# Performance work log

Measured on AMD Instinct MI355X. Metric: run time of the kernel, lower is better.

The kernel has to match this reference:

```python
import jax, jax.numpy as jnp
import numpy as np
import math

B, N, E, H = 2, 10000, 160000, 128
ET = 8
EPS = 1e-5


def setup_inputs() -> dict:
    key = jax.random.key(0)
    ks = jax.random.split(key, 20)
    s = 1.0 / math.sqrt(H)
    inp = {
        "hidden": jax.random.normal(ks[0], (B, N, H), jnp.float32),
        "time_emb": jax.random.normal(ks[1], (B, N, H), jnp.float32),
        "edge_index": jax.random.randint(ks[2], (2, E), 0, N),
        "edge_type": jax.random.randint(ks[3], (E,), 0, ET),
        # parameters
        "edge_emb": jax.random.normal(ks[4], (ET, H), jnp.float32),
        "Wq": jax.random.normal(ks[5], (H, H), jnp.float32) * s,
        "bq": jnp.zeros((H,), jnp.float32),
        "Wk": jax.random.normal(ks[6], (H, H), jnp.float32) * s,
        "bk": jnp.zeros((H,), jnp.float32),
        "Wv": jax.random.normal(ks[7], (H, H), jnp.float32) * s,
        "bv": jnp.zeros((H,), jnp.float32),
        "We": jax.random.normal(ks[8], (H, 1), jnp.float32) * s,
        "be": jnp.zeros((1,), jnp.float32),
        "W1": jax.random.normal(ks[9], (3 * H, H), jnp.float32) * (1.0 / math.sqrt(3 * H)),
        "b1": jnp.zeros((H,), jnp.float32),
        "W2": jax.random.normal(ks[10], (H, H), jnp.float32) * s,
        "b2": jnp.zeros((H,), jnp.float32),
        "gamma": jnp.ones((H,), jnp.float32),
        "beta": jnp.zeros((H,), jnp.float32),
    }
    return inp


def _forward(hidden, time_emb, edge_index, edge_type, edge_emb,
             Wq, bq, Wk, bk, Wv, bv, We, be, W1, b1, W2, b2, gamma, beta):
    src, tgt = edge_index[0], edge_index[1]
    # edge-wise gathers: [B, E, H]
    src_h = hidden[:, src]
    tgt_h = hidden[:, tgt]
    src_t = time_emb[:, src]
    tgt_t = time_emb[:, tgt]
    edge_h = edge_emb[edge_type][None, :, :]  # [1, E, H] broadcasts over batch

    query = (tgt_h + tgt_t) @ Wq + bq
    key = (src_h + src_t + edge_h) @ Wk + bk
    value = (src_h + edge_h) @ Wv + bv

    logits = jnp.einsum("beh,beh->be", query, key) / math.sqrt(H)
    logits = logits + (edge_h @ We + be)[..., 0]  # edge bias broadcast over batch

    # segment softmax per target node (equivalent to the per-node masked softmax loop)
    lT = logits.T  # [E, B]
    seg_max = jax.ops.segment_max(lT, tgt, num_segments=N)          # [N, B]
    seg_max = jnp.where(jnp.isfinite(seg_max), seg_max, 0.0)
    ex = jnp.exp(lT - seg_max[tgt])                                  # [E, B]
    seg_sum = jax.ops.segment_sum(ex, tgt, num_segments=N)           # [N, B]
    weights = (ex / seg_sum[tgt]).T                                  # [B, E]

    messages = value * weights[..., None]                            # [B, E, H]
    # scatter-add to target nodes
    agg = jax.ops.segment_sum(jnp.swapaxes(messages, 0, 1), tgt, num_segments=N)  # [N, B, H]
    aggregated = jnp.swapaxes(agg, 0, 1)                             # [B, N, H]

    cat = jnp.concatenate([hidden, aggregated, time_emb], axis=-1)   # [B, N, 3H]
    updated = jax.nn.silu(cat @ W1 + b1) @ W2 + b2

    x = hidden + updated  # dropout p=0 -> identity
    mu = jnp.mean(x, axis=-1, keepdims=True)
    var = jnp.var(x, axis=-1, keepdims=True)
    return (x - mu) * jax.lax.rsqrt(var + EPS) * gamma + beta


def reference(hidden, time_emb, edge_index, edge_type, edge_emb,
              Wq, bq, Wk, bk, Wv, bv, We, be, W1, b1, W2, b2, gamma, beta):
    return _forward(hidden, time_emb, edge_index, edge_type, edge_emb,
                    Wq, bq, Wk, bk, Wv, bv, We, be, W1, b1, W2, b2, gamma, beta)
```

## Files before the change

### kernel.cpp

```cpp
#include <hip/hip_runtime.h>
#include <math.h>

constexpr int B_  = 2;
constexpr int N_  = 10000;
constexpr int E_  = 160000;
constexpr int H_  = 128;
constexpr int ET_ = 8;
constexpr int CAP_ = 64;
constexpr float EPS_ = 1e-5f;
constexpr float RSQH = 0.08838834764831845f;

typedef __bf16 bf16x8 __attribute__((ext_vector_type(8)));
typedef short  short8 __attribute__((ext_vector_type(8)));
typedef float  f32x4  __attribute__((ext_vector_type(4)));
typedef unsigned short u16;

__device__ inline u16 bf16b(float f) {
    return __builtin_bit_cast(u16, (__bf16)f);
}

__device__ inline bf16x8 ldfrag(const u16* __restrict__ W, int kc, int nt, int lane) {
    short8 s = *(const short8*)(W + ((kc * 8 + nt) * 64 + lane) * 8);
    return __builtin_bit_cast(bf16x8, s);
}

__global__ __launch_bounds__(256)
void setup_kernel(const float* __restrict__ W1, const float* __restrict__ W2,
                  const float* __restrict__ Wq, const float* __restrict__ Wk,
                  const float* __restrict__ Wv,
                  u16* __restrict__ W1s, u16* __restrict__ W2s,
                  u16* __restrict__ Wqs, u16* __restrict__ Wks, u16* __restrict__ Wvs,
                  const float* __restrict__ edge_emb,
                  const float* __restrict__ bk, const float* __restrict__ bv,
                  const float* __restrict__ We, const float* __restrict__ be,
                  float* __restrict__ Kt, float* __restrict__ Vt, float* __restrict__ eb,
                  int* __restrict__ count)
{
    const int bid = blockIdx.x, tid = threadIdx.x;
    if (bid < 56) {
        int unit = bid >> 1, half = bid & 1;
        const float* src; u16* dst; int kc;
        if (unit < 12)      { src = W1; dst = W1s; kc = unit; }
        else if (unit < 16) { src = W2; dst = W2s; kc = unit - 12; }
        else if (unit < 20) { src = Wq; dst = Wqs; kc = unit - 16; }
        else if (unit < 24) { src = Wk; dst = Wks; kc = unit - 20; }
        else                { src = Wv; dst = Wvs; kc = unit - 24; }
        int nt = half * 4 + (tid >> 6), lane = tid & 63;
        int q = lane >> 4, c = lane & 15;
        int kbase = kc * 32 + q * 8;
        int col = nt * 16 + c;
        u16* out = dst + ((kc * 8 + nt) * 64 + lane) * 8;
#pragma unroll
        for (int j = 0; j < 8; ++j)
            out[j] = bf16b(src[(kbase + j) * H_ + col]);
    } else if (bid < 64) {
        int t = bid - 56;
        const float* ep = edge_emb + t * H_;
        __shared__ float red[2];
        int j = tid;
        if (j < 128) {
            float ak = bk[j], av = bv[j];
            for (int d = 0; d < H_; d += 4) {
                float e0 = ep[d], e1 = ep[d+1], e2 = ep[d+2], e3 = ep[d+3];
                ak += e0*Wk[(d+0)*H_+j] + e1*Wk[(d+1)*H_+j] + e2*Wk[(d+2)*H_+j] + e3*Wk[(d+3)*H_+j];
                av += e0*Wv[(d+0)*H_+j] + e1*Wv[(d+1)*H_+j] + e2*Wv[(d+2)*H_+j] + e3*Wv[(d+3)*H_+j];
            }
            Kt[t*H_ + j] = ak;
            Vt[t*H_ + j] = av;
            float pe = ep[j] * We[j];
#pragma unroll
            for (int off = 32; off; off >>= 1) pe += __shfl_xor(pe, off);
            if ((j & 63) == 0) red[j >> 6] = pe;
        }
        __syncthreads();
        if (j == 0) eb[t] = red[0] + red[1] + be[0];
    } else {
        int i0 = (bid - 64) * 1024;
        for (int i = i0 + tid; i < i0 + 1024; i += 256)
            if (i < N_) count[i] = 0;
    }
}

__global__ __launch_bounds__(256)
void scatter_qkv_kernel(const int* __restrict__ src, const int* __restrict__ tgt,
                        const int* __restrict__ type, int* __restrict__ count,
                        int* __restrict__ slots,
                        const float* __restrict__ hidden, const float* __restrict__ time_emb,
                        const u16* __restrict__ Wqs, const u16* __restrict__ Wks,
                        const u16* __restrict__ Wvs, const float* __restrict__ bq,
                        u16* __restrict__ Q, u16* __restrict__ KV)
{
    if (blockIdx.x < 625) {
        int e = blockIdx.x * 256 + threadIdx.x;
        if (e < E_) {
            int t = tgt[e];
            int pos = atomicAdd(&count[t], 1);
            slots[t * CAP_ + pos] = src[e] | (type[e] << 16);
        }
        return;
    }
    const int wv = threadIdx.x >> 6, lane = threadIdx.x & 63;
    const int tile = (blockIdx.x - 625) * 4 + wv;
    if (tile >= (B_ * N_) / 16) return;
    const int nbase = tile * 16;
    const int m = lane & 15, q = lane >> 4;
    const int koff = q * 8;

    bf16x8 aq[4], av[4];
    const float* hp = hidden   + (nbase + m) * H_ + koff;
    const float* tp = time_emb + (nbase + m) * H_ + koff;
#pragma unroll
    for (int kc = 0; kc < 4; ++kc) {
        float4 h0 = *(const float4*)(hp + kc * 32);
        float4 h1 = *(const float4*)(hp + kc * 32 + 4);
        float4 t0 = *(const float4*)(tp + kc * 32);
        float4 t1 = *(const float4*)(tp + kc * 32 + 4);
        bf16x8 fv, fq;
        fv[0]=(__bf16)h0.x; fv[1]=(__bf16)h0.y; fv[2]=(__bf16)h0.z; fv[3]=(__bf16)h0.w;
        fv[4]=(__bf16)h1.x; fv[5]=(__bf16)h1.y; fv[6]=(__bf16)h1.z; fv[7]=(__bf16)h1.w;
        fq[0]=(__bf16)(h0.x+t0.x); fq[1]=(__bf16)(h0.y+t0.y);
        fq[2]=(__bf16)(h0.z+t0.z); fq[3]=(__bf16)(h0.w+t0.w);
        fq[4]=(__bf16)(h1.x+t1.x); fq[5]=(__bf16)(h1.y+t1.y);
        fq[6]=(__bf16)(h1.z+t1.z); fq[7]=(__bf16)(h1.w+t1.w);
        av[kc] = fv; aq[kc] = fq;
    }

    f32x4 accq[8], acck[8], accv[8];
#pragma unroll
    for (int nt = 0; nt < 8; ++nt) { accq[nt] = (f32x4)0.f; acck[nt] = (f32x4)0.f; accv[nt] = (f32x4)0.f; }

#pragma unroll
    for (int kc = 0; kc < 4; ++kc) {
#pragma unroll
        for (int nt = 0; nt < 8; ++nt) {
            bf16x8 bfq = ldfrag(Wqs, kc, nt, lane);
            bf16x8 bfk = ldfrag(Wks, kc, nt, lane);
            bf16x8 bfv = ldfrag(Wvs, kc, nt, lane);
            accq[nt] = __builtin_amdgcn_mfma_f32_16x16x32_bf16(aq[kc], bfq, accq[nt], 0, 0, 0);
            acck[nt] = __builtin_amdgcn_mfma_f32_16x16x32_bf16(aq[kc], bfk, acck[nt], 0, 0, 0);
            accv[nt] = __builtin_amdgcn_mfma_f32_16x16x32_bf16(av[kc], bfv, accv[nt], 0, 0, 0);
        }
    }

#pragma unroll
    for (int nt = 0; nt < 8; ++nt) {
        int col = nt * 16 + m;
        float bqc = bq[col];
#pragma unroll
        for (int r = 0; r < 4; ++r) {
            int node = nbase + q * 4 + r;
            Q[(size_t)node * H_ + col] = bf16b(accq[nt][r] + bqc);
            KV[(size_t)node * 256 + col]       = bf16b(acck[nt][r]);
            KV[(size_t)node * 256 + 128 + col] = bf16b(accv[nt][r]);
        }
    }
}

__global__ __launch_bounds__(256)
void attn_kernel(const u16* __restrict__ Qb, const u16* __restrict__ KV,
                 const float* __restrict__ Kt, const float* __restrict__ Vt,
                 const float* __restrict__ eb,
                 const int* __restrict__ count, const int* __restrict__ slots,
                 u16* __restrict__ aggb)
{
    __shared__ float bias_s[4][2][8];
    __shared__ __align__(16) u16 vt_s[8][128];

    const int tid = threadIdx.x;
    const int wv = tid >> 6, lane = tid & 63;
    const int g = lane >> 4, lam = lane & 15;

    for (int idx = tid; idx < ET_ * H_; idx += 256)
        vt_s[idx >> 7][idx & 127] = bf16b(Vt[idx]);
    __syncthreads();

    const int n = blockIdx.x * 4 + wv;
    const int cnt = count[n];
    const int sbase = n * CAP_;
    const u16* __restrict__ KV0 = KV;
    const u16* __restrict__ KV1 = KV + (size_t)N_ * 256;

    int myslot = 0;
    {
        int idx = g + 4 * lam;
        if (idx < cnt) myslot = slots[sbase + idx];
    }
    const int lb = lane & 48;

    float q0[8], q1[8];
    {
        short8 sa = *(const short8*)(Qb + (size_t)n * H_ + lam * 8);
        short8 sb = *(const short8*)(Qb + (size_t)(N_ + n) * H_ + lam * 8);
        bf16x8 qa = __builtin_bit_cast(bf16x8, sa);
        bf16x8 qb = __builtin_bit_cast(bf16x8, sb);
#pragma unroll
        for (int j = 0; j < 8; ++j) { q0[j] = (float)qa[j]; q1[j] = (float)qb[j]; }
    }

    {
        const float* k0p = Kt + (2 * g) * H_ + lam * 8;
        const float* k1p = Kt + (2 * g + 1) * H_ + lam * 8;
        float p00 = 0.f, p01 = 0.f, p10 = 0.f, p11 = 0.f;
#pragma unroll
        for (int j = 0; j < 8; ++j) {
            float ka = k0p[j], kb = k1p[j];
            p00 += q0[j] * ka; p01 += q0[j] * kb;
            p10 += q1[j] * ka; p11 += q1[j] * kb;
        }
#pragma unroll
        for (int msk = 1; msk < 16; msk <<= 1) {
            p00 += __shfl_xor(p00, msk);
            p01 += __shfl_xor(p01, msk);
            p10 += __shfl_xor(p10, msk);
            p11 += __shfl_xor(p11, msk);
        }
        if (lam == 0) {
            bias_s[wv][0][2 * g]     = p00 * RSQH + eb[2 * g];
            bias_s[wv][0][2 * g + 1] = p01 * RSQH + eb[2 * g + 1];
            bias_s[wv][1][2 * g]     = p10 * RSQH + eb[2 * g];
            bias_s[wv][1][2 * g + 1] = p11 * RSQH + eb[2 * g + 1];
        }
    }

    float m0 = -INFINITY, l0 = 0.f, m1 = -INFINITY, l1 = 0.f;
    float acc0[8], acc1[8];
#pragma unroll
    for (int j = 0; j < 8; ++j) { acc0[j] = 0.f; acc1[j] = 0.f; }

    int c = g;
    for (; c + 4 < cnt; c += 8) {
        int r = (c - g) >> 2;
        int pkA = __shfl(myslot, lb + r);
        int pkB = __shfl(myslot, lb + r + 1);
        int sA = pkA & 0xFFFF, tA = pkA >> 16;
        int sB = pkB & 0xFFFF, tB = pkB >> 16;
        short8 k0A = *(const short8*)(KV0 + (size_t)sA * 256 + lam * 8);
        short8 k0B = *(const short8*)(KV0 + (size_t)sB * 256 + lam * 8);
        short8 k1A = *(const short8*)(KV1 + (size_t)sA * 256 + lam * 8);
        short8 k1B = *(const short8*)(KV1 + (size_t)sB * 256 + lam * 8);
        short8 v0A = *(const short8*)(KV0 + (size_t)sA * 256 + 128 + lam * 8);
        short8 v0B = *(const short8*)(KV0 + (size_t)sB * 256 + 128 + lam * 8);
        short8 v1A = *(const short8*)(KV1 + (size_t)sA * 256 + 128 + lam * 8);
        short8 v1B = *(const short8*)(KV1 + (size_t)sB * 256 + 128 + lam * 8);
        short8 vtA = *(const short8*)(&vt_s[tA][lam * 8]);
        short8 vtB = *(const short8*)(&vt_s[tB][lam * 8]);
        bf16x8 ka0A = __builtin_bit_cast(bf16x8, k0A);
        bf16x8 ka0B = __builtin_bit_cast(bf16x8, k0B);
        bf16x8 ka1A = __builtin_bit_cast(bf16x8, k1A);
        bf16x8 ka1B = __builtin_bit_cast(bf16x8, k1B);
        float d0A = 0.f, d0B = 0.f, d1A = 0.f, d1B = 0.f;
#pragma unroll
        for (int j = 0; j < 8; ++j) {
            d0A += q0[j] * (float)ka0A[j];
            d0B += q0[j] * (float)ka0B[j];
            d1A += q1[j] * (float)ka1A[j];
            d1B += q1[j] * (float)ka1B[j];
        }
#pragma unroll
        for (int msk = 1; msk < 16; msk <<= 1) {
            d0A += __shfl_xor(d0A, msk);
            d0B += __shfl_xor(d0B, msk);
            d1A += __shfl_xor(d1A, msk);
            d1B += __shfl_xor(d1B, msk);
        }
        float lg0A = d0A * RSQH + bias_s[wv][0][tA];
        float lg0B = d0B * RSQH + bias_s[wv][0][tB];
        float lg1A = d1A * RSQH + bias_s[wv][1][tA];
        float lg1B = d1B * RSQH + bias_s[wv][1][tB];
        bf16x8 va0A = __builtin_bit_cast(bf16x8, v0A);
        bf16x8 va0B = __builtin_bit_cast(bf16x8, v0B);
        bf16x8 va1A = __builtin_bit_cast(bf16x8, v1A);
        bf16x8 va1B = __builtin_bit_cast(bf16x8, v1B);
        bf16x8 vtaA = __builtin_bit_cast(bf16x8, vtA);
        bf16x8 vtaB = __builtin_bit_cast(bf16x8, vtB);
        {
            float mx = fmaxf(lg0A, lg0B);
            if (mx > m0 + 8.f) {
                float rs = __expf(m0 - mx);
                l0 *= rs;
#pragma unroll
                for (int j = 0; j < 8; ++j) acc0[j] *= rs;
                m0 = mx;
            }
            float wA = __expf(lg0A - m0);
            float wB = __expf(lg0B - m0);
            l0 += wA + wB;
#pragma unroll
            for (int j = 0; j < 8; ++j)
                acc0[j] += wA * ((float)va0A[j] + (float)vtaA[j])
                         + wB * ((float)va0B[j] + (float)vtaB[j]);
        }
        {
            float mx = fmaxf(lg1A, lg1B);
            if (mx > m1 + 8.f) {
                float rs = __expf(m1 - mx);
                l1 *= rs;
#pragma unroll
                for (int j = 0; j < 8; ++j) acc1[j] *= rs;
                m1 = mx;
            }
            float wA = __expf(lg1A - m1);
            float wB = __expf(lg1B - m1);
            l1 += wA + wB;
#pragma unroll
            for (int j = 0; j < 8; ++j)
                acc1[j] += wA * ((float)va1A[j] + (float)vtaA[j])
                         + wB * ((float)va1B[j] + (float)vtaB[j]);
        }
    }
    if (c < cnt) {
        int r = (c - g) >> 2;
        int pkA = __shfl(myslot, lb + r);
        int sA = pkA & 0xFFFF, tA = pkA >> 16;
        short8 k0A = *(const short8*)(KV0 + (size_t)sA * 256 + lam * 8);
        short8 k1A = *(const short8*)(KV1 + (size_t)sA * 256 + lam * 8);
        short8 v0A = *(const short8*)(KV0 + (size_t)sA * 256 + 128 + lam * 8);
        short8 v1A = *(const short8*)(KV1 + (size_t)sA * 256 + 128 + lam * 8);
        short8 vtA = *(const short8*)(&vt_s[tA][lam * 8]);
        bf16x8 ka0A = __builtin_bit_cast(bf16x8, k0A);
        bf16x8 ka1A = __builtin_bit_cast(bf16x8, k1A);
        float d0A = 0.f, d1A = 0.f;
#pragma unroll
        for (int j = 0; j < 8; ++j) {
            d0A += q0[j] * (float)ka0A[j];
            d1A += q1[j] * (float)ka1A[j];
        }
#pragma unroll
        for (int msk = 1; msk < 16; msk <<= 1) {
            d0A += __shfl_xor(d0A, msk);
            d1A += __shfl_xor(d1A, msk);
        }
        float lg0A = d0A * RSQH + bias_s[wv][0][tA];
        float lg1A = d1A * RSQH + bias_s[wv][1][tA];
        bf16x8 va0A = __builtin_bit_cast(bf16x8, v0A);
        bf16x8 va1A = __builtin_bit_cast(bf16x8, v1A);
        bf16x8 vtaA = __builtin_bit_cast(bf16x8, vtA);
        if (lg0A > m0 + 8.f) {
            float rs = __expf(m0 - lg0A);
            l0 *= rs;
#pragma unroll
            for (int j = 0; j < 8; ++j) acc0[j] *= rs;
            m0 = lg0A;
        }
        float w0 = __expf(lg0A - m0);
        l0 += w0;
#pragma unroll
        for (int j = 0; j < 8; ++j)
            acc0[j] += w0 * ((float)va0A[j] + (float)vtaA[j]);
        if (lg1A > m1 + 8.f) {
            float rs = __expf(m1 - lg1A);
            l1 *= rs;
#pragma unroll
            for (int j = 0; j < 8; ++j) acc1[j] *= rs;
            m1 = lg1A;
        }
        float w1 = __expf(lg1A - m1);
        l1 += w1;
#pragma unroll
        for (int j = 0; j < 8; ++j)
            acc1[j] += w1 * ((float)va1A[j] + (float)vtaA[j]);
    }

    {
        float M = fmaxf(m0, __shfl_xor(m0, 16));
        M = fmaxf(M, __shfl_xor(M, 32));
        float rs = (m0 == M) ? 1.f : __expf(m0 - M);
        l0 *= rs;
#pragma unroll
        for (int j = 0; j < 8; ++j) {
            acc0[j] *= rs;
            acc0[j] += __shfl_xor(acc0[j], 16);
            acc0[j] += __shfl_xor(acc0[j], 32);
        }
        l0 += __shfl_xor(l0, 16);
        l0 += __shfl_xor(l0, 32);
    }
    {
        float M = fmaxf(m1, __shfl_xor(m1, 16));
        M = fmaxf(M, __shfl_xor(M, 32));
        float rs = (m1 == M) ? 1.f : __expf(m1 - M);
        l1 *= rs;
#pragma unroll
        for (int j = 0; j < 8; ++j) {
            acc1[j] *= rs;
            acc1[j] += __shfl_xor(acc1[j], 16);
            acc1[j] += __shfl_xor(acc1[j], 32);
        }
        l1 += __shfl_xor(l1, 16);
        l1 += __shfl_xor(l1, 32);
    }

    if (g == 0) {
        float invL0 = (cnt > 0) ? 1.f / l0 : 0.f;
        float invL1 = (cnt > 0) ? 1.f / l1 : 0.f;
        bf16x8 o0, o1;
#pragma unroll
        for (int j = 0; j < 8; ++j) {
            o0[j] = (__bf16)(acc0[j] * invL0);
            o1[j] = (__bf16)(acc1[j] * invL1);
        }
        *(short8*)(aggb + (size_t)n * H_ + lam * 8)        = __builtin_bit_cast(short8, o0);
        *(short8*)(aggb + (size_t)(N_ + n) * H_ + lam * 8) = __builtin_bit_cast(short8, o1);
    }
}

__global__ __launch_bounds__(256)
void mlp_mfma_kernel(const float* __restrict__ hidden, const u16* __restrict__ aggb,
                     const float* __restrict__ time_emb,
                     const u16* __restrict__ W1s, const u16* __restrict__ W2s,
                     const float* __restrict__ b1, const float* __restrict__ b2,
                     const float* __restrict__ gamma, const float* __restrict__ beta,
                     float* __restrict__ out)
{
    __shared__ __align__(16) u16 h1s[4][16][136];
    const int wv = threadIdx.x >> 6, lane = threadIdx.x & 63;
    const int tile = blockIdx.x * 4 + wv;
    if (tile >= (B_ * N_) / 16) return;
    const int nbase = tile * 16;
    const int m = lane & 15, q = lane >> 4;
    const int koff = q * 8;

    bf16x8 a[12];
    const float* hp = hidden   + (nbase + m) * H_ + koff;
    const float* tp = time_emb + (nbase + m) * H_ + koff;
    const u16*   ap = aggb + (size_t)(nbase + m) * H_ + koff;
#pragma unroll
    for (int kc = 0; kc < 4; ++kc) {
        float4 h0 = *(const float4*)(hp + kc * 32);
        float4 h1 = *(const float4*)(hp + kc * 32 + 4);
        float4 t0 = *(const float4*)(tp + kc * 32);
        float4 t1 = *(const float4*)(tp + kc * 32 + 4);
        bf16x8 fh, ft;
        fh[0]=(__bf16)h0.x; fh[1]=(__bf16)h0.y; fh[2]=(__bf16)h0.z; fh[3]=(__bf16)h0.w;
        fh[4]=(__bf16)h1.x; fh[5]=(__bf16)h1.y; fh[6]=(__bf16)h1.z; fh[7]=(__bf16)h1.w;
        ft[0]=(__bf16)t0.x; ft[1]=(__bf16)t0.y; ft[2]=(__bf16)t0.z; ft[3]=(__bf16)t0.w;
        ft[4]=(__bf16)t1.x; ft[5]=(__bf16)t1.y; ft[6]=(__bf16)t1.z; ft[7]=(__bf16)t1.w;
        a[0 * 4 + kc] = fh;
        a[2 * 4 + kc] = ft;
        short8 s8 = *(const short8*)(ap + kc * 32);
        a[1 * 4 + kc] = __builtin_bit_cast(bf16x8, s8);
    }

    f32x4 acc[8];
#pragma unroll
    for (int nt = 0; nt < 8; ++nt) acc[nt] = (f32x4)0.f;
#pragma unroll
    for (int kc = 0; kc < 12; ++kc) {
#pragma unroll
        for (int nt = 0; nt < 8; ++nt) {
            bf16x8 bf = ldfrag(W1s, kc, nt, lane);
            acc[nt] = __builtin_amdgcn_mfma_f32_16x16x32_bf16(a[kc], bf, acc[nt], 0, 0, 0);
        }
    }

#pragma unroll
    for (int nt = 0; nt < 8; ++nt) {
        int col = nt * 16 + m;
        float bb = b1[col];
#pragma unroll
        for (int r = 0; r < 4; ++r) {
            float v = acc[nt][r] + bb;
            float h = v / (1.f + __expf(-v));
            h1s[wv][q * 4 + r][col] = bf16b(h);
        }
    }

    f32x4 acc2[8];
#pragma unroll
    for (int nt = 0; nt < 8; ++nt) acc2[nt] = (f32x4)0.f;
#pragma unroll
    for (int kc = 0; kc < 4; ++kc) {
        short8 s8 = *(const short8*)&h1s[wv][m][kc * 32 + koff];
        bf16x8 a2 = __builtin_bit_cast(bf16x8, s8);
#pragma unroll
        for (int nt = 0; nt < 8; ++nt) {
            bf16x8 bf = ldfrag(W2s, kc, nt, lane);
            acc2[nt] = __builtin_amdgcn_mfma_f32_16x16x32_bf16(a2, bf, acc2[nt], 0, 0, 0);
        }
    }

    float x[8][4];
#pragma unroll
    for (int nt = 0; nt < 8; ++nt) {
        int col = nt * 16 + m;
        float bb = b2[col];
#pragma unroll
        for (int r = 0; r < 4; ++r) {
            int node = nbase + q * 4 + r;
            x[nt][r] = hidden[node * H_ + col] + acc2[nt][r] + bb;
        }
    }
#pragma unroll
    for (int r = 0; r < 4; ++r) {
        float s = 0.f, ss = 0.f;
#pragma unroll
        for (int nt = 0; nt < 8; ++nt) { s += x[nt][r]; ss += x[nt][r] * x[nt][r]; }
#pragma unroll
        for (int off = 1; off < 16; off <<= 1) {
            s  += __shfl_xor(s, off);
            ss += __shfl_xor(ss, off);
        }
        float mu  = s * (1.f / H_);
        float var = ss * (1.f / H_) - mu * mu;
        float rs  = rsqrtf(var + EPS_);
        int node = nbase + q * 4 + r;
#pragma unroll
        for (int nt = 0; nt < 8; ++nt) {
            int col = nt * 16 + m;
            out[node * H_ + col] = (x[nt][r] - mu) * rs * gamma[col] + beta[col];
        }
    }
}

extern "C" void kernel_launch(void* const* d_in, const int* in_sizes, int n_in,
                              void* d_out, int out_size, void* d_ws, size_t ws_size,
                              hipStream_t stream)
{
    const float* hidden   = (const float*)d_in[0];
    const float* time_emb = (const float*)d_in[1];
    const int*   eidx     = (const int*)d_in[2];
    const int*   etype    = (const int*)d_in[3];
    const float* edge_emb = (const float*)d_in[4];
    const float* Wq = (const float*)d_in[5];
    const float* bq = (const float*)d_in[6];
    const float* Wk = (const float*)d_in[7];
    const float* bk = (const float*)d_in[8];
    const float* Wv = (const float*)d_in[9];
    const float* bv = (const float*)d_in[10];
    const float* We = (const float*)d_in[11];
    const float* be = (const float*)d_in[12];
    const float* W1 = (const float*)d_in[13];
    const float* b1 = (const float*)d_in[14];
    const float* W2 = (const float*)d_in[15];
    const float* b2 = (const float*)d_in[16];
    const float* gamma = (const float*)d_in[17];
    const float* beta  = (const float*)d_in[18];
    float* out = (float*)d_out;

    constexpr int BNH = B_ * N_ * H_;
    u16* Qb   = (u16*)d_ws;
    u16* KVb  = Qb + BNH;
    u16* aggb = KVb + (size_t)B_ * N_ * 256;
    float* Kt  = (float*)(aggb + BNH);
    float* Vt  = Kt + ET_ * H_;
    float* ebt = Vt + ET_ * H_;
    int* count = (int*)(ebt + ET_);
    int* slots = count + N_;
    uintptr_t wp = (uintptr_t)(slots + N_ * CAP_);
    wp = (wp + 15) & ~(uintptr_t)15;
    u16* W1s = (u16*)wp;
    u16* W2s = W1s + 384 * 128;
    u16* Wqs = W2s + 128 * 128;
    u16* Wks = Wqs + 128 * 128;
    u16* Wvs = Wks + 128 * 128;

    const int* esrc = eidx;
    const int* etgt = eidx + E_;

    setup_kernel<<<74, 256, 0, stream>>>(
        W1, W2, Wq, Wk, Wv, W1s, W2s, Wqs, Wks, Wvs,
        edge_emb, bk, bv, We, be, Kt, Vt, ebt, count);
    scatter_qkv_kernel<<<625 + 313, 256, 0, stream>>>(
        esrc, etgt, etype, count, slots,
        hidden, time_emb, Wqs, Wks, Wvs, bq, Qb, KVb);
    attn_kernel<<<N_ / 4, 256, 0, stream>>>(
        Qb, KVb, Kt, Vt, ebt, count, slots, aggb);
    mlp_mfma_kernel<<<313, 256, 0, stream>>>(
        hidden, aggb, time_emb, W1s, W2s, b1, b2, gamma, beta, out);
}
```

Measured before the change: 173.7 us.

## Split MLP tile across eight waves, one output column block per wave

The MLP kernel previously assigned one 16-node tile per wave, with each wave computing all 8 output column blocks. Now each 512-thread block handles one tile and each of its 8 waves computes one 16-column block. The hidden activations are shared through LDS with a barrier, and the LayerNorm statistics are reduced across waves through shared memory. The aim is more parallelism (1250 blocks instead of 313) and lower register pressure. The cost is that every wave redundantly loads and converts the full A fragments, and extra syncs are added.

```diff
diff --git a/kernel.cpp b/kernel.cpp
--- a/kernel.cpp
+++ b/kernel.cpp
@@ -179,13 +179,13 @@
     const int sbase = n * CAP_;
     const u16* __restrict__ KV0 = KV;
     const u16* __restrict__ KV1 = KV + (size_t)N_ * 256;
+    const int lb = lane & 48;
 
     int myslot = 0;
     {
         int idx = g + 4 * lam;
         if (idx < cnt) myslot = slots[sbase + idx];
     }
-    const int lb = lane & 48;
 
     float q0[8], q1[8];
     {
@@ -404,7 +404,7 @@
     }
 }
 
-__global__ __launch_bounds__(256)
+__global__ __launch_bounds__(512)
 void mlp_mfma_kernel(const float* __restrict__ hidden, const u16* __restrict__ aggb,
                      const float* __restrict__ time_emb,
                      const u16* __restrict__ W1s, const u16* __restrict__ W2s,
@@ -412,17 +412,16 @@
                      const float* __restrict__ gamma, const float* __restrict__ beta,
                      float* __restrict__ out)
 {
-    __shared__ __align__(16) u16 h1s[4][16][136];
+    __shared__ __align__(16) u16 h1s[16][136];
+    __shared__ float sp[16][8], ssp[16][8];
     const int wv = threadIdx.x >> 6, lane = threadIdx.x & 63;
-    const int tile = blockIdx.x * 4 + wv;
-    if (tile >= (B_ * N_) / 16) return;
-    const int nbase = tile * 16;
+    const int nbase = blockIdx.x * 16;
     const int m = lane & 15, q = lane >> 4;
     const int koff = q * 8;
 
     bf16x8 a[12];
-    const float* hp = hidden   + (nbase + m) * H_ + koff;
-    const float* tp = time_emb + (nbase + m) * H_ + koff;
+    const float* hp = hidden   + (size_t)(nbase + m) * H_ + koff;
+    const float* tp = time_emb + (size_t)(nbase + m) * H_ + koff;
     const u16*   ap = aggb + (size_t)(nbase + m) * H_ + koff;
 #pragma unroll
     for (int kc = 0; kc < 4; ++kc) {
@@ -441,73 +440,70 @@
         a[1 * 4 + kc] = __builtin_bit_cast(bf16x8, s8);
     }
 
-    f32x4 acc[8];
-#pragma unroll
-    for (int nt = 0; nt < 8; ++nt) acc[nt] = (f32x4)0.f;
+    f32x4 acc1 = (f32x4)0.f;
 #pragma unroll
     for (int kc = 0; kc < 12; ++kc) {
-#pragma unroll
-        for (int nt = 0; nt < 8; ++nt) {
-            bf16x8 bf = ldfrag(W1s, kc, nt, lane);
-            acc[nt] = __builtin_amdgcn_mfma_f32_16x16x32_bf16(a[kc], bf, acc[nt], 0, 0, 0);
-        }
-    }
-
-#pragma unroll
-    for (int nt = 0; nt < 8; ++nt) {
-        int col = nt * 16 + m;
+        bf16x8 bf = ldfrag(W1s, kc, wv, lane);
+        acc1 = __builtin_amdgcn_mfma_f32_16x16x32_bf16(a[kc], bf, acc1, 0, 0, 0);
+    }
+    {
+        int col = wv * 16 + m;
         float bb = b1[col];
 #pragma unroll
         for (int r = 0; r < 4; ++r) {
-            float v = acc[nt][r] + bb;
+            float v = acc1[r] + bb;
             float h = v / (1.f + __expf(-v));
-            h1s[wv][q * 4 + r][col] = bf16b(h);
-        }
-    }
-
-    f32x4 acc2[8];
-#pragma unroll
-    for (int nt = 0; nt < 8; ++nt) acc2[nt] = (f32x4)0.f;
+            h1s[q * 4 + r][col] = bf16b(h);
+        }
+    }
+    __syncthreads();
+
+    f32x4 acc2 = (f32x4)0.f;
 #pragma unroll
     for (int kc = 0; kc < 4; ++kc) {
-        short8 s8 = *(const short8*)&h1s[wv][m][kc * 32 + koff];
+        short8 s8 = *(const short8*)(&h1s[m][kc * 32 + koff]);
         bf16x8 a2 = __builtin_bit_cast(bf16x8, s8);
-#pragma unroll
-        for (int nt = 0; nt < 8; ++nt) {
-            bf16x8 bf = ldfrag(W2s, kc, nt, lane);
-            acc2[nt] = __builtin_amdgcn_mfma_f32_16x16x32_bf16(a2, bf, acc2[nt], 0, 0, 0);
-        }
-    }
-
-    float x[8][4];
-#pragma unroll
-    for (int nt = 0; nt < 8; ++nt) {
-        int col = nt * 16 + m;
+        bf16x8 bf = ldfrag(W2s, kc, wv, lane);
+        acc2 = __builtin_amdgcn_mfma_f32_16x16x32_bf16(a2, bf, acc2, 0, 0, 0);
+    }
+
+    float x[4];
+    {
+        int col = wv * 16 + m;
         float bb = b2[col];
 #pragma unroll
         for (int r = 0; r < 4; ++r) {
             int node = nbase + q * 4 + r;
-            x[nt][r] = hidden[node * H_ + col] + acc2[nt][r] + bb;
+            x[r] = hidden[(size_t)node * H_ + col] + acc2[r] + bb;
         }
     }
 #pragma unroll
     for (int r = 0; r < 4; ++r) {
-        float s = 0.f, ss = 0.f;
-#pragma unroll
-        for (int nt = 0; nt < 8; ++nt) { s += x[nt][r]; ss += x[nt][r] * x[nt][r]; }
+        float s  = x[r];
+        float ss = x[r] * x[r];
 #pragma unroll
         for (int off = 1; off < 16; off <<= 1) {
             s  += __shfl_xor(s, off);
             ss += __shfl_xor(ss, off);
         }
-        float mu  = s * (1.f / H_);
-        float var = ss * (1.f / H_) - mu * mu;
-        float rs  = rsqrtf(var + EPS_);
-        int node = nbase + q * 4 + r;
-#pragma unroll
-        for (int nt = 0; nt < 8; ++nt) {
-            int col = nt * 16 + m;
-            out[node * H_ + col] = (x[nt][r] - mu) * rs * gamma[col] + beta[col];
+        if (m == 0) { sp[q * 4 + r][wv] = s; ssp[q * 4 + r][wv] = ss; }
+    }
+    __syncthreads();
+
+    {
+        int col = wv * 16 + m;
+#pragma unroll
+        for (int r = 0; r < 4; ++r) {
+            int nl = q * 4 + r;
+            float s  = (sp[nl][0]  + sp[nl][1])  + (sp[nl][2]  + sp[nl][3])
+                     + (sp[nl][4]  + sp[nl][5])  + (sp[nl][6]  + sp[nl][7]);
+            float ss = (ssp[nl][0] + ssp[nl][1]) + (ssp[nl][2] + ssp[nl][3])
+                     + (ssp[nl][4] + ssp[nl][5]) + (ssp[nl][6] + ssp[nl][7]);
+            float mu  = s * (1.f / H_);
+            float var = ss * (1.f / H_) - mu * mu;
+            float rsn = rsqrtf(var + EPS_);
+            int node = nbase + nl;
+            out[(size_t)node * H_ + col] = (x[r] - mu) * rsn * gamma[col] + beta[col];
         }
     }
 }
@@ -565,6 +561,6 @@
         hidden, time_emb, Wqs, Wks, Wvs, bq, Qb, KVb);
     attn_kernel<<<N_ / 4, 256, 0, stream>>>(
         Qb, KVb, Kt, Vt, ebt, count, slots, aggb);
-    mlp_mfma_kernel<<<313, 256, 0, stream>>>(
+    mlp_mfma_kernel<<<(B_ * N_) / 16, 512, 0, stream>>>(
         hidden, aggb, time_emb, W1s, W2s, b1, b2, gamma, beta, out);
 }
```

Result: slower. 185.3 us (+6.7%).
